# Performance work log

Measured on AMD Instinct MI355X. Metric: run time of the kernel, lower is better.

## Reference

```python
import jax, jax.numpy as jnp
import numpy as np

N_NODES = 50000
N_EDGES = 800000
IN_CH = 128
HIDDEN = 16
HEADS = 8
OUT_CH = 128
EDGE_DIM = 16


def _lin_params(key, fan_in, fan_out, bias=True):
    k1, k2 = jax.random.split(key)
    s = 1.0 / np.sqrt(fan_in)
    W = jax.random.uniform(k1, (fan_in, fan_out), jnp.float32, -s, s)
    if bias:
        b = jax.random.uniform(k2, (fan_out,), jnp.float32, -s, s)
        return W, b
    return W


def setup_inputs() -> dict:
    key = jax.random.key(0)
    ks = jax.random.split(key, 16)
    x = jax.random.normal(ks[0], (N_NODES, IN_CH), jnp.float32)
    edge_index = jax.random.randint(ks[1], (2, N_EDGES), 0, N_NODES, jnp.int64)
    edge_attr = jax.random.normal(ks[2], (N_EDGES, EDGE_DIM), jnp.float32)
    HC0 = HEADS * HIDDEN
    Wq0, bq0 = _lin_params(ks[3], IN_CH, HC0)
    Wk0, bk0 = _lin_params(ks[4], IN_CH, HC0)
    Wv0, bv0 = _lin_params(ks[5], IN_CH, HC0)
    We0 = _lin_params(ks[6], EDGE_DIM, HC0, bias=False)
    Ws0, bs0 = _lin_params(ks[7], IN_CH, HC0)
    Wq1, bq1 = _lin_params(ks[8], HC0, OUT_CH)
    Wk1, bk1 = _lin_params(ks[9], HC0, OUT_CH)
    Wv1, bv1 = _lin_params(ks[10], HC0, OUT_CH)
    We1 = _lin_params(ks[11], EDGE_DIM, OUT_CH, bias=False)
    Ws1, bs1 = _lin_params(ks[12], HC0, OUT_CH)
    return dict(x=x, edge_index=edge_index, edge_attr=edge_attr,
                Wq0=Wq0, bq0=bq0, Wk0=Wk0, bk0=bk0, Wv0=Wv0, bv0=bv0, We0=We0, Ws0=Ws0, bs0=bs0,
                Wq1=Wq1, bq1=bq1, Wk1=Wk1, bk1=bk1, Wv1=Wv1, bv1=bv1, We1=We1, Ws1=Ws1, bs1=bs1)


def transformer_conv(x, src, dst, edge_attr, Wq, bq, Wk, bk, Wv, bv, We, Ws, bs, heads, concat):
    """PyG TransformerConv: gather-attend-softmax(per dst)-scatter, edge features added to key/value."""
    N = x.shape[0]
    E = src.shape[0]
    C = Wq.shape[1] // heads
    q = (x @ Wq + bq).reshape(N, heads, C)
    k = (x @ Wk + bk).reshape(N, heads, C)
    v = (x @ Wv + bv).reshape(N, heads, C)
    e = (edge_attr @ We).reshape(E, heads, C)
    key_e = k[src] + e                                  # [E,H,C]
    alpha = jnp.sum(q[dst] * key_e, axis=-1) / jnp.sqrt(jnp.asarray(C, x.dtype))  # [E,H]
    # segment softmax over incoming edges of each dst node
    m = jax.ops.segment_max(alpha, dst, num_segments=N)       # [N,H]
    p = jnp.exp(alpha - m[dst])
    denom = jax.ops.segment_sum(p, dst, num_segments=N)       # [N,H]
    w = p / (denom[dst] + 1e-16)                              # [E,H]
    msg = (v[src] + e) * w[..., None]                         # [E,H,C]
    agg = jax.ops.segment_sum(msg.reshape(E, heads * C), dst, num_segments=N).reshape(N, heads, C)
    out = agg.reshape(N, heads * C) if concat else agg.mean(axis=1)
    return out + (x @ Ws + bs)                                # root skip connection


def reference(x, edge_index, edge_attr,
              Wq0, bq0, Wk0, bk0, Wv0, bv0, We0, Ws0, bs0,
              Wq1, bq1, Wk1, bk1, Wv1, bv1, We1, Ws1, bs1):
    src, dst = edge_index[0], edge_index[1]
    h = transformer_conv(x, src, dst, edge_attr, Wq0, bq0, Wk0, bk0, Wv0, bv0, We0, Ws0, bs0,
                         heads=HEADS, concat=True)
    h = jax.nn.relu(h)
    out = transformer_conv(h, src, dst, edge_attr, Wq1, bq1, Wk1, bk1, Wv1, bv1, We1, Ws1, bs1,
                           heads=1, concat=False)
    return out
```

## Files before the change

### kernel.cpp

```cpp
#include <hip/hip_runtime.h>
#include <stdint.h>

#define N_NODES 50000
#define N_EDGES 800000

typedef __bf16 bf16x8 __attribute__((ext_vector_type(8)));
typedef float f32x4 __attribute__((ext_vector_type(4)));

__device__ __forceinline__ unsigned short f2bf(float f) {
  union { float f; unsigned int i; } x; x.f = f;
  unsigned int i = x.i;
  unsigned int r = (i + 0x7fffu + ((i >> 16) & 1u)) >> 16;
  return (unsigned short)r;
}
__device__ __forceinline__ float bfl(unsigned int p) {
  union { unsigned int i; float f; } x; x.i = p << 16; return x.f;
}
__device__ __forceinline__ float bfh(unsigned int p) {
  union { unsigned int i; float f; } x; x.i = p & 0xffff0000u; return x.f;
}

struct Ptr8 { const float* p[8]; };

__global__ __launch_bounds__(256) void transpose_w(Ptr8 ws, unsigned short* wt) {
  int mat = blockIdx.x;
  const float* W = ws.p[mat];
  unsigned short* out = wt + mat * 16384;
  for (int it = 0; it < 64; ++it) {
    int idx = it * 256 + threadIdx.x;
    int n = idx >> 7, k = idx & 127;
    out[n * 128 + k] = f2bf(W[k * 128 + n]);
  }
}

__global__ void zero_kernel(int* cnt, int* cursor, int* srcpad, unsigned int* eapad) {
  int i = blockIdx.x * blockDim.x + threadIdx.x;
  if (i < N_NODES) { cnt[i] = 0; cursor[i] = 0; }
  if (i < 8)  srcpad[i] = 0;
  if (i < 64) eapad[i] = 0;
}

__global__ void hist_kernel(const int* __restrict__ dst, int* __restrict__ cnt) {
  int e = blockIdx.x * blockDim.x + threadIdx.x;
  if (e < N_EDGES) atomicAdd(&cnt[dst[e]], 1);
}

__global__ __launch_bounds__(1024) void scan_kernel(const int* __restrict__ cnt, int* __restrict__ rs) {
  const int n = N_NODES, per = 49;
  int t = threadIdx.x;
  int lo = t * per; int hi = lo + per;
  if (lo > n) lo = n;
  if (hi > n) hi = n;
  int s = 0;
  for (int i = lo; i < hi; ++i) s += cnt[i];
  int lane = t & 63, wv = t >> 6;
  int v = s;
  #pragma unroll
  for (int off = 1; off < 64; off <<= 1) {
    int u = __shfl_up(v, off, 64);
    if (lane >= off) v += u;
  }
  __shared__ int wsum[16], woff[16];
  if (lane == 63) wsum[wv] = v;
  __syncthreads();
  if (t == 0) { int a = 0; for (int w = 0; w < 16; ++w) { woff[w] = a; a += wsum[w]; } }
  __syncthreads();
  int run = woff[wv] + (v - s);
  if (t == 0) rs[0] = 0;
  for (int i = lo; i < hi; ++i) { run += cnt[i]; rs[i + 1] = run; }
}

__global__ void scatter_kernel(const int* __restrict__ src, const int* __restrict__ dst,
                               const int* __restrict__ rs, int* __restrict__ cursor,
                               int* __restrict__ srcArr, int* __restrict__ eidxArr) {
  int e = blockIdx.x * blockDim.x + threadIdx.x;
  if (e < N_EDGES) {
    int d = dst[e];
    int pos = rs[d] + atomicAdd(&cursor[d], 1);
    srcArr[pos]  = src[e];
    eidxArr[pos] = e;
  }
}

__global__ __launch_bounds__(256) void ea_gather(const float* __restrict__ EA,
                                                 const int* __restrict__ eidxArr,
                                                 unsigned short* __restrict__ eacsr) {
  int r = blockIdx.x * 32 + (threadIdx.x >> 3);
  if (r >= N_EDGES) return;
  int j = (threadIdx.x & 7) * 2;
  int e = eidxArr[r];
  float2 v = *(const float2*)(EA + (size_t)e * 16 + j);
  unsigned int pk = (unsigned int)f2bf(v.x) | ((unsigned int)f2bf(v.y) << 16);
  *(unsigned int*)(eacsr + (size_t)r * 16 + j) = pk;
}

struct Gemm4Args {
  const float* Xf;
  const unsigned short* Xh;
  const unsigned short* Wt;
  const float* b[4];
  unsigned short* o[4];
  int M;
};

template<bool XF32>
__global__ __launch_bounds__(256) void node_gemm4(Gemm4Args ga) {
  __shared__ alignas(16) unsigned short At[128 * 128];
  __shared__ alignas(16) unsigned short Bt[128 * 128];
  int m0 = blockIdx.x * 128;
  int lane = threadIdx.x & 63, wv = threadIdx.x >> 6;
  int wm = wv >> 1, wn = wv & 1;
  int lr = lane & 15, lk = lane >> 4;

  #pragma unroll
  for (int it = 0; it < 8; ++it) {
    int c = it * 256 + threadIdx.x;
    int row = c >> 4, slot = c & 15;
    int dsl = slot ^ (row & 7);
    int grow = m0 + row; if (grow >= ga.M) grow = ga.M - 1;
    alignas(16) unsigned short tmp[8];
    if (XF32) {
      const float* xp = ga.Xf + (size_t)grow * 128 + slot * 8;
      float4 a = *(const float4*)xp;
      float4 b = *(const float4*)(xp + 4);
      tmp[0] = f2bf(a.x); tmp[1] = f2bf(a.y); tmp[2] = f2bf(a.z); tmp[3] = f2bf(a.w);
      tmp[4] = f2bf(b.x); tmp[5] = f2bf(b.y); tmp[6] = f2bf(b.z); tmp[7] = f2bf(b.w);
    } else {
      *(uint4*)tmp = *(const uint4*)(ga.Xh + (size_t)grow * 128 + slot * 8);
    }
    *(uint4*)(&At[row * 128 + dsl * 8]) = *(const uint4*)tmp;
  }

  #pragma unroll
  for (int which = 0; which < 4; ++which) {
    if (which) __syncthreads();
    const unsigned short* Wt = ga.Wt + which * 16384;
    #pragma unroll
    for (int it = 0; it < 8; ++it) {
      int c = it * 256 + threadIdx.x;
      int row = c >> 4, slot = c & 15;
      int dsl = slot ^ (row & 7);
      *(uint4*)(&Bt[row * 128 + dsl * 8]) = *(const uint4*)(Wt + c * 8);
    }
    __syncthreads();

    f32x4 acc[4][4];
    #pragma unroll
    for (int mi = 0; mi < 4; ++mi)
      #pragma unroll
      for (int ni = 0; ni < 4; ++ni) acc[mi][ni] = (f32x4){0.f, 0.f, 0.f, 0.f};

    #pragma unroll
    for (int kk = 0; kk < 4; ++kk) {
      bf16x8 af[4], bfr[4];
      #pragma unroll
      for (int mi = 0; mi < 4; ++mi) {
        int row = wm * 64 + mi * 16 + lr;
        int slot = (kk * 4 + lk) ^ (row & 7);
        af[mi] = *(const bf16x8*)(&At[row * 128 + slot * 8]);
      }
      #pragma unroll
      for (int ni = 0; ni < 4; ++ni) {
        int row = wn * 64 + ni * 16 + lr;
        int slot = (kk * 4 + lk) ^ (row & 7);
        bfr[ni] = *(const bf16x8*)(&Bt[row * 128 + slot * 8]);
      }
      #pragma unroll
      for (int mi = 0; mi < 4; ++mi)
        #pragma unroll
        for (int ni = 0; ni < 4; ++ni)
          acc[mi][ni] = __builtin_amdgcn_mfma_f32_16x16x32_bf16(af[mi], bfr[ni], acc[mi][ni], 0, 0, 0);
    }

    const float* bias = ga.b[which];
    unsigned short* outp = ga.o[which];
    float bv[4];
    #pragma unroll
    for (int ni = 0; ni < 4; ++ni) bv[ni] = bias[wn * 64 + ni * 16 + lr];
    #pragma unroll
    for (int mi = 0; mi < 4; ++mi) {
      #pragma unroll
      for (int i = 0; i < 4; ++i) {
        int row = m0 + wm * 64 + mi * 16 + lk * 4 + i;
        if (row < ga.M) {
          #pragma unroll
          for (int ni = 0; ni < 4; ++ni) {
            int col = wn * 64 + ni * 16 + lr;
            outp[(size_t)row * 128 + col] = f2bf(acc[mi][ni][i] + bv[ni]);
          }
        }
      }
    }
  }
}

template<int CHALF, bool RELU, bool OUT_BF16>
__global__ __launch_bounds__(256) void edge_attn(
    const unsigned short* __restrict__ Q, const unsigned short* __restrict__ Kb,
    const unsigned short* __restrict__ Vb, const unsigned short* __restrict__ S,
    const float* __restrict__ We, const unsigned short* __restrict__ EAC,
    const int* __restrict__ srcArr, const int* __restrict__ rs,
    void* __restrict__ outv, float inv_sqrt_c) {
  int wv = threadIdx.x >> 6, lane = threadIdx.x & 63;
  int node = blockIdx.x * 4 + wv;
  if (node >= N_NODES) return;
  int c0 = lane * 2;
  int jbase = (lane & 1) * 8 + ((lane >> 1) & 1) * 4 + ((lane >> 2) & 1) * 2;

  unsigned int qp = *(const unsigned int*)(Q + (size_t)node * 128 + c0);
  unsigned int sp = *(const unsigned int*)(S + (size_t)node * 128 + c0);
  float qa = bfl(qp) * inv_sqrt_c;
  float qb = bfh(qp) * inv_sqrt_c;

  float part[16];
  #pragma unroll
  for (int j = 0; j < 16; ++j) {
    float2 wp = *(const float2*)(We + j * 128 + c0);
    part[j] = qa * wp.x + qb * wp.y;
  }
  {
    bool hi = lane & 1;
    #pragma unroll
    for (int j = 0; j < 8; ++j) {
      float kept = hi ? part[j + 8] : part[j];
      float sent = hi ? part[j] : part[j + 8];
      part[j] = kept + __shfl_xor(sent, 1, 64);
    }
    hi = lane & 2;
    #pragma unroll
    for (int j = 0; j < 4; ++j) {
      float kept = hi ? part[j + 4] : part[j];
      float sent = hi ? part[j] : part[j + 4];
      part[j] = kept + __shfl_xor(sent, 2, 64);
    }
    hi = lane & 4;
    #pragma unroll
    for (int j = 0; j < 2; ++j) {
      float kept = hi ? part[j + 2] : part[j];
      float sent = hi ? part[j] : part[j + 2];
      part[j] = kept + __shfl_xor(sent, 4, 64);
    }
  }
  if (CHALF == 64) {
    #pragma unroll
    for (int s = 8; s <= 32; s <<= 1) {
      part[0] += __shfl_xor(part[0], s, 64);
      part[1] += __shfl_xor(part[1], s, 64);
    }
  }
  float qw0 = part[0] * (CHALF == 64 ? 0.125f : 1.0f);
  float qw1 = part[1] * (CHALF == 64 ? 0.125f : 1.0f);

  int i0 = rs[node], i1 = rs[node + 1];
  int deg = i1 - i0;
  float den = 0.f, a0 = 0.f, a1 = 0.f, wea0 = 0.f, wea1 = 0.f;

  struct Buf { unsigned int kp[8], vp[8], ep[8]; };
  Buf bA, bB;
  int svA = 0, svB = 0;

  auto load_src = [&](int c) -> int {
    return srcArr[i0 + c * 8 + (lane & 7)];
  };
  auto gather = [&](Buf& b, int c, int sv) {
    #pragma unroll
    for (int j = 0; j < 8; ++j) {
      int s = __shfl(sv, j, 8);
      b.kp[j] = *(const unsigned int*)(Kb + (size_t)s * 128 + c0);
      b.vp[j] = *(const unsigned int*)(Vb + (size_t)s * 128 + c0);
      b.ep[j] = *(const unsigned int*)(EAC + (size_t)(i0 + c * 8 + j) * 16 + jbase);
    }
  };
  auto compute = [&](const Buf& b, int c) {
    #pragma unroll
    for (int j = 0; j < 8; ++j) {
      int g = i0 + c * 8 + j;
      float ea0 = bfl(b.ep[j]), ea1 = bfh(b.ep[j]);
      float p = qa * bfl(b.kp[j]) + qb * bfh(b.kp[j]) + qw0 * ea0 + qw1 * ea1;
      #pragma unroll
      for (int off = 1; off < CHALF; off <<= 1) p += __shfl_xor(p, off, 64);
      float w = (g < i1) ? __expf(p) : 0.f;
      den  += w;
      a0   += w * bfl(b.vp[j]);
      a1   += w * bfh(b.vp[j]);
      wea0 += w * ea0;
      wea1 += w * ea1;
    }
  };

  int nch = (deg + 7) >> 3;
  if (nch > 0) {
    svA = load_src(0);
    if (nch > 1) svB = load_src(1);
    gather(bA, 0, svA);
    int c = 0;
    while (true) {
      if (c + 1 < nch) gather(bB, c + 1, svB);
      if (c + 2 < nch) svA = load_src(c + 2);
      compute(bA, c);
      ++c; if (c >= nch) break;
      if (c + 1 < nch) gather(bA, c + 1, svA);
      if (c + 2 < nch) svB = load_src(c + 2);
      compute(bB, c);
      ++c; if (c >= nch) break;
    }
  }

  float inv = 1.f / (den + 1e-16f);
  float eadd0 = 0.f, eadd1 = 0.f;
  #pragma unroll
  for (int j = 0; j < 16; ++j) {
    int owner = ((j >> 3) & 1) | (((j >> 2) & 1) << 1) | (((j >> 1) & 1) << 2);
    int srcl = (lane & 56) | owner;
    float val = __shfl((j & 1) ? wea1 : wea0, srcl, 64);
    float2 wp = *(const float2*)(We + j * 128 + c0);
    eadd0 += val * wp.x;
    eadd1 += val * wp.y;
  }
  float o0 = (a0 + eadd0) * inv + bfl(sp);
  float o1 = (a1 + eadd1) * inv + bfh(sp);
  if (RELU) { o0 = fmaxf(o0, 0.f); o1 = fmaxf(o1, 0.f); }
  if (OUT_BF16) {
    unsigned int op = ((unsigned int)f2bf(o1) << 16) | (unsigned int)f2bf(o0);
    *(unsigned int*)((unsigned short*)outv + (size_t)node * 128 + c0) = op;
  } else {
    *(float2*)((float*)outv + (size_t)node * 128 + c0) = make_float2(o0, o1);
  }
}

extern "C" void kernel_launch(void* const* d_in, const int* in_sizes, int n_in,
                              void* d_out, int out_size, void* d_ws, size_t ws_size,
                              hipStream_t stream) {
  const float* x   = (const float*)d_in[0];
  const int*   ei  = (const int*)d_in[1];
  const float* ea  = (const float*)d_in[2];
  const float* Wq0 = (const float*)d_in[3];
  const float* bq0 = (const float*)d_in[4];
  const float* Wk0 = (const float*)d_in[5];
  const float* bk0 = (const float*)d_in[6];
  const float* Wv0 = (const float*)d_in[7];
  const float* bv0 = (const float*)d_in[8];
  const float* We0 = (const float*)d_in[9];
  const float* Ws0 = (const float*)d_in[10];
  const float* bs0 = (const float*)d_in[11];
  const float* Wq1 = (const float*)d_in[12];
  const float* bq1 = (const float*)d_in[13];
  const float* Wk1 = (const float*)d_in[14];
  const float* bk1 = (const float*)d_in[15];
  const float* Wv1 = (const float*)d_in[16];
  const float* bv1 = (const float*)d_in[17];
  const float* We1 = (const float*)d_in[18];
  const float* Ws1 = (const float*)d_in[19];
  const float* bs1 = (const float*)d_in[20];

  char* ws = (char*)d_ws;
  size_t off = 0;
  auto alloc = [&](size_t bytes) -> void* {
    void* p = ws + off;
    off = (off + bytes + 255) & ~(size_t)255;
    return p;
  };
  unsigned short* WT    = (unsigned short*)alloc(8 * 16384 * 2);
  unsigned short* q     = (unsigned short*)alloc((size_t)N_NODES * 128 * 2);
  unsigned short* k     = (unsigned short*)alloc((size_t)N_NODES * 128 * 2);
  unsigned short* v     = (unsigned short*)alloc((size_t)N_NODES * 128 * 2);
  unsigned short* s     = (unsigned short*)alloc((size_t)N_NODES * 128 * 2);
  unsigned short* h     = (unsigned short*)alloc((size_t)N_NODES * 128 * 2);
  unsigned short* eacsr = (unsigned short*)alloc(((size_t)N_EDGES + 8) * 16 * 2);
  int* cnt     = (int*)alloc(N_NODES * 4);
  int* rs      = (int*)alloc((N_NODES + 1) * 4);
  int* cursor  = (int*)alloc(N_NODES * 4);
  int* srcArr  = (int*)alloc(((size_t)N_EDGES + 8) * 4);
  int* eidxArr = (int*)alloc((size_t)N_EDGES * 4);

  const int* srcp = ei;
  const int* dstp = ei + N_EDGES;

  Ptr8 p8 = {{Wq0, Wk0, Wv0, Ws0, Wq1, Wk1, Wv1, Ws1}};
  transpose_w<<<8, 256, 0, stream>>>(p8, WT);
  zero_kernel<<<196, 256, 0, stream>>>(cnt, cursor, srcArr + N_EDGES,
                                       (unsigned int*)(eacsr + (size_t)N_EDGES * 16));
  hist_kernel<<<3125, 256, 0, stream>>>(dstp, cnt);
  scan_kernel<<<1, 1024, 0, stream>>>(cnt, rs);
  scatter_kernel<<<3125, 256, 0, stream>>>(srcp, dstp, rs, cursor, srcArr, eidxArr);
  ea_gather<<<25000, 256, 0, stream>>>(ea, eidxArr, eacsr);

  Gemm4Args ga0 = { x, nullptr, WT, {bq0, bk0, bv0, bs0}, {q, k, v, s}, N_NODES };
  node_gemm4<true><<<391, 256, 0, stream>>>(ga0);
  edge_attn<8, true, true><<<12500, 256, 0, stream>>>(q, k, v, s, We0, eacsr,
                                                      srcArr, rs, h, 0.25f);

  Gemm4Args ga1 = { nullptr, h, WT + 4 * 16384, {bq1, bk1, bv1, bs1}, {q, k, v, s}, N_NODES };
  node_gemm4<false><<<391, 256, 0, stream>>>(ga1);
  edge_attn<64, false, false><<<12500, 256, 0, stream>>>(q, k, v, s, We1, eacsr,
                                                         srcArr, rs, d_out, 0.08838834764831845f);
}
```

Measured before the change: 639.0 us.

## Interleave K/V rows, fuse edge-attr gather into scatter, persistent attention grid

The GEMM epilogue now writes K and V interleaved into one buffer, so each edge gather in the attention kernel is a single 8-byte load per lane instead of two 4-byte loads. Edge-attribute bf16 conversion is folded into the CSR scatter kernel, which removes the separate ea_gather pass and the eidx array. The zero kernel is replaced by memsets. The attention kernel becomes a grid-stride loop over 2048 blocks with an occupancy hint, and it moves the EA and S loads to later in the loop. The costs are scattered 2-byte stores in the GEMM epilogue and edge-attr loads that are no longer prefetched.

```diff
diff --git a/kernel.cpp b/kernel.cpp
--- a/kernel.cpp
+++ b/kernel.cpp
@@ -3,6 +3,7 @@
 
 #define N_NODES 50000
 #define N_EDGES 800000
+#define NGROUPS ((N_NODES + 3) / 4)
 
 typedef __bf16 bf16x8 __attribute__((ext_vector_type(8)));
 typedef float f32x4 __attribute__((ext_vector_type(4)));
@@ -12,6 +13,9 @@
   unsigned int i = x.i;
   unsigned int r = (i + 0x7fffu + ((i >> 16) & 1u)) >> 16;
   return (unsigned short)r;
+}
+__device__ __forceinline__ unsigned int pk2bf(float a, float b) {
+  return (unsigned int)f2bf(a) | ((unsigned int)f2bf(b) << 16);
 }
 __device__ __forceinline__ float bfl(unsigned int p) {
   union { unsigned int i; float f; } x; x.i = p << 16; return x.f;
@@ -31,13 +35,6 @@
     int n = idx >> 7, k = idx & 127;
     out[n * 128 + k] = f2bf(W[k * 128 + n]);
   }
-}
-
-__global__ void zero_kernel(int* cnt, int* cursor, int* srcpad, unsigned int* eapad) {
-  int i = blockIdx.x * blockDim.x + threadIdx.x;
-  if (i < N_NODES) { cnt[i] = 0; cursor[i] = 0; }
-  if (i < 8)  srcpad[i] = 0;
-  if (i < 64) eapad[i] = 0;
 }
 
 __global__ void hist_kernel(const int* __restrict__ dst, int* __restrict__ cnt) {
@@ -71,27 +68,21 @@
 }
 
 __global__ void scatter_kernel(const int* __restrict__ src, const int* __restrict__ dst,
+                               const float* __restrict__ EA,
                                const int* __restrict__ rs, int* __restrict__ cursor,
-                               int* __restrict__ srcArr, int* __restrict__ eidxArr) {
+                               int* __restrict__ srcArr, unsigned short* __restrict__ eacsr) {
   int e = blockIdx.x * blockDim.x + threadIdx.x;
   if (e < N_EDGES) {
     int d = dst[e];
     int pos = rs[d] + atomicAdd(&cursor[d], 1);
-    srcArr[pos]  = src[e];
-    eidxArr[pos] = e;
-  }
-}
-
-__global__ __launch_bounds__(256) void ea_gather(const float* __restrict__ EA,
-                                                 const int* __restrict__ eidxArr,
-                                                 unsigned short* __restrict__ eacsr) {
-  int r = blockIdx.x * 32 + (threadIdx.x >> 3);
-  if (r >= N_EDGES) return;
-  int j = (threadIdx.x & 7) * 2;
-  int e = eidxArr[r];
-  float2 v = *(const float2*)(EA + (size_t)e * 16 + j);
-  unsigned int pk = (unsigned int)f2bf(v.x) | ((unsigned int)f2bf(v.y) << 16);
-  *(unsigned int*)(eacsr + (size_t)r * 16 + j) = pk;
+    srcArr[pos] = src[e];
+    const float4* p = (const float4*)(EA + (size_t)e * 16);
+    float4 r0 = p[0], r1 = p[1], r2 = p[2], r3 = p[3];
+    uint4 u0 = { pk2bf(r0.x, r0.y), pk2bf(r0.z, r0.w), pk2bf(r1.x, r1.y), pk2bf(r1.z, r1.w) };
+    uint4 u1 = { pk2bf(r2.x, r2.y), pk2bf(r2.z, r2.w), pk2bf(r3.x, r3.y), pk2bf(r3.z, r3.w) };
+    *(uint4*)(eacsr + (size_t)pos * 16) = u0;
+    *(uint4*)(eacsr + (size_t)pos * 16 + 8) = u1;
+  }
 }
 
 struct Gemm4Args {
@@ -99,7 +90,9 @@
   const unsigned short* Xh;
   const unsigned short* Wt;
   const float* b[4];
-  unsigned short* o[4];
+  unsigned short* qb;
+  unsigned short* kvb;
+  unsigned short* sb;
   int M;
 };
 
@@ -173,7 +166,6 @@
     }
 
     const float* bias = ga.b[which];
-    unsigned short* outp = ga.o[which];
     float bv[4];
     #pragma unroll
     for (int ni = 0; ni < 4; ++ni) bv[ni] = bias[wn * 64 + ni * 16 + lr];
@@ -186,7 +178,10 @@
           #pragma unroll
           for (int ni = 0; ni < 4; ++ni) {
             int col = wn * 64 + ni * 16 + lr;
-            outp[(size_t)row * 128 + col] = f2bf(acc[mi][ni][i] + bv[ni]);
+            unsigned short val = f2bf(acc[mi][ni][i] + bv[ni]);
+            if (which == 0)      ga.qb[(size_t)row * 128 + col] = val;
+            else if (which == 3) ga.sb[(size_t)row * 128 + col] = val;
+            else ga.kvb[(size_t)row * 256 + (size_t)(col >> 1) * 4 + (col & 1) + (which == 2 ? 2 : 0)] = val;
           }
         }
       }
@@ -195,136 +190,138 @@
 }
 
 template<int CHALF, bool RELU, bool OUT_BF16>
-__global__ __launch_bounds__(256) void edge_attn(
-    const unsigned short* __restrict__ Q, const unsigned short* __restrict__ Kb,
-    const unsigned short* __restrict__ Vb, const unsigned short* __restrict__ S,
-    const float* __restrict__ We, const unsigned short* __restrict__ EAC,
+__global__ __launch_bounds__(256, 8) void edge_attn(
+    const unsigned short* __restrict__ Q, const uint2* __restrict__ KV,
+    const unsigned short* __restrict__ S, const float* __restrict__ We,
+    const unsigned short* __restrict__ EAC,
     const int* __restrict__ srcArr, const int* __restrict__ rs,
     void* __restrict__ outv, float inv_sqrt_c) {
   int wv = threadIdx.x >> 6, lane = threadIdx.x & 63;
-  int node = blockIdx.x * 4 + wv;
-  if (node >= N_NODES) return;
   int c0 = lane * 2;
   int jbase = (lane & 1) * 8 + ((lane >> 1) & 1) * 4 + ((lane >> 2) & 1) * 2;
 
-  unsigned int qp = *(const unsigned int*)(Q + (size_t)node * 128 + c0);
-  unsigned int sp = *(const unsigned int*)(S + (size_t)node * 128 + c0);
-  float qa = bfl(qp) * inv_sqrt_c;
-  float qb = bfh(qp) * inv_sqrt_c;
-
-  float part[16];
-  #pragma unroll
-  for (int j = 0; j < 16; ++j) {
-    float2 wp = *(const float2*)(We + j * 128 + c0);
-    part[j] = qa * wp.x + qb * wp.y;
-  }
-  {
-    bool hi = lane & 1;
-    #pragma unroll
-    for (int j = 0; j < 8; ++j) {
-      float kept = hi ? part[j + 8] : part[j];
-      float sent = hi ? part[j] : part[j + 8];
-      part[j] = kept + __shfl_xor(sent, 1, 64);
-    }
-    hi = lane & 2;
-    #pragma unroll
-    for (int j = 0; j < 4; ++j) {
-      float kept = hi ? part[j + 4] : part[j];
-      float sent = hi ? part[j] : part[j + 4];
-      part[j] = kept + __shfl_xor(sent, 2, 64);
-    }
-    hi = lane & 4;
-    #pragma unroll
-    for (int j = 0; j < 2; ++j) {
-      float kept = hi ? part[j + 2] : part[j];
-      float sent = hi ? part[j] : part[j + 2];
-      part[j] = kept + __shfl_xor(sent, 4, 64);
-    }
-  }
-  if (CHALF == 64) {
-    #pragma unroll
-    for (int s = 8; s <= 32; s <<= 1) {
-      part[0] += __shfl_xor(part[0], s, 64);
-      part[1] += __shfl_xor(part[1], s, 64);
-    }
-  }
-  float qw0 = part[0] * (CHALF == 64 ? 0.125f : 1.0f);
-  float qw1 = part[1] * (CHALF == 64 ? 0.125f : 1.0f);
-
-  int i0 = rs[node], i1 = rs[node + 1];
-  int deg = i1 - i0;
-  float den = 0.f, a0 = 0.f, a1 = 0.f, wea0 = 0.f, wea1 = 0.f;
-
-  struct Buf { unsigned int kp[8], vp[8], ep[8]; };
-  Buf bA, bB;
-  int svA = 0, svB = 0;
-
-  auto load_src = [&](int c) -> int {
-    return srcArr[i0 + c * 8 + (lane & 7)];
-  };
-  auto gather = [&](Buf& b, int c, int sv) {
-    #pragma unroll
-    for (int j = 0; j < 8; ++j) {
-      int s = __shfl(sv, j, 8);
-      b.kp[j] = *(const unsigned int*)(Kb + (size_t)s * 128 + c0);
-      b.vp[j] = *(const unsigned int*)(Vb + (size_t)s * 128 + c0);
-      b.ep[j] = *(const unsigned int*)(EAC + (size_t)(i0 + c * 8 + j) * 16 + jbase);
-    }
-  };
-  auto compute = [&](const Buf& b, int c) {
-    #pragma unroll
-    for (int j = 0; j < 8; ++j) {
-      int g = i0 + c * 8 + j;
-      float ea0 = bfl(b.ep[j]), ea1 = bfh(b.ep[j]);
-      float p = qa * bfl(b.kp[j]) + qb * bfh(b.kp[j]) + qw0 * ea0 + qw1 * ea1;
-      #pragma unroll
-      for (int off = 1; off < CHALF; off <<= 1) p += __shfl_xor(p, off, 64);
-      float w = (g < i1) ? __expf(p) : 0.f;
-      den  += w;
-      a0   += w * bfl(b.vp[j]);
-      a1   += w * bfh(b.vp[j]);
-      wea0 += w * ea0;
-      wea1 += w * ea1;
-    }
-  };
-
-  int nch = (deg + 7) >> 3;
-  if (nch > 0) {
-    svA = load_src(0);
-    if (nch > 1) svB = load_src(1);
-    gather(bA, 0, svA);
-    int c = 0;
-    while (true) {
-      if (c + 1 < nch) gather(bB, c + 1, svB);
-      if (c + 2 < nch) svA = load_src(c + 2);
-      compute(bA, c);
-      ++c; if (c >= nch) break;
-      if (c + 1 < nch) gather(bA, c + 1, svA);
-      if (c + 2 < nch) svB = load_src(c + 2);
-      compute(bB, c);
-      ++c; if (c >= nch) break;
-    }
-  }
-
-  float inv = 1.f / (den + 1e-16f);
-  float eadd0 = 0.f, eadd1 = 0.f;
-  #pragma unroll
-  for (int j = 0; j < 16; ++j) {
-    int owner = ((j >> 3) & 1) | (((j >> 2) & 1) << 1) | (((j >> 1) & 1) << 2);
-    int srcl = (lane & 56) | owner;
-    float val = __shfl((j & 1) ? wea1 : wea0, srcl, 64);
-    float2 wp = *(const float2*)(We + j * 128 + c0);
-    eadd0 += val * wp.x;
-    eadd1 += val * wp.y;
-  }
-  float o0 = (a0 + eadd0) * inv + bfl(sp);
-  float o1 = (a1 + eadd1) * inv + bfh(sp);
-  if (RELU) { o0 = fmaxf(o0, 0.f); o1 = fmaxf(o1, 0.f); }
-  if (OUT_BF16) {
-    unsigned int op = ((unsigned int)f2bf(o1) << 16) | (unsigned int)f2bf(o0);
-    *(unsigned int*)((unsigned short*)outv + (size_t)node * 128 + c0) = op;
-  } else {
-    *(float2*)((float*)outv + (size_t)node * 128 + c0) = make_float2(o0, o1);
+  for (int ng = blockIdx.x; ng < NGROUPS; ng += gridDim.x) {
+    int node = ng * 4 + wv;
+    if (node >= N_NODES) continue;
+
+    unsigned int qp = *(const unsigned int*)(Q + (size_t)node * 128 + c0);
+    float qa = bfl(qp) * inv_sqrt_c;
+    float qb = bfh(qp) * inv_sqrt_c;
+
+    float part[16];
+    #pragma unroll
+    for (int j = 0; j < 16; ++j) {
+      float2 wp = *(const float2*)(We + j * 128 + c0);
+      part[j] = qa * wp.x + qb * wp.y;
+    }
+    {
+      bool hi = lane & 1;
+      #pragma unroll
+      for (int j = 0; j < 8; ++j) {
+        float kept = hi ? part[j + 8] : part[j];
+        float sent = hi ? part[j] : part[j + 8];
+        part[j] = kept + __shfl_xor(sent, 1, 64);
+      }
+      hi = lane & 2;
+      #pragma unroll
+      for (int j = 0; j < 4; ++j) {
+        float kept = hi ? part[j + 4] : part[j];
+        float sent = hi ? part[j] : part[j + 4];
+        part[j] = kept + __shfl_xor(sent, 2, 64);
+      }
+      hi = lane & 4;
+      #pragma unroll
+      for (int j = 0; j < 2; ++j) {
+        float kept = hi ? part[j + 2] : part[j];
+        float sent = hi ? part[j] : part[j + 2];
+        part[j] = kept + __shfl_xor(sent, 4, 64);
+      }
+    }
+    if (CHALF == 64) {
+      #pragma unroll
+      for (int s = 8; s <= 32; s <<= 1) {
+        part[0] += __shfl_xor(part[0], s, 64);
+        part[1] += __shfl_xor(part[1], s, 64);
+      }
+    }
+    float qw0 = part[0] * (CHALF == 64 ? 0.125f : 1.0f);
+    float qw1 = part[1] * (CHALF == 64 ? 0.125f : 1.0f);
+
+    int i0 = rs[node], i1 = rs[node + 1];
+    int deg = i1 - i0;
+    float den = 0.f, a0 = 0.f, a1 = 0.f, wea0 = 0.f, wea1 = 0.f;
+
+    struct Buf { uint2 kv[8]; };
+    Buf bA, bB;
+    int svA = 0, svB = 0;
+
+    auto load_src = [&](int c) -> int {
+      return srcArr[i0 + c * 8 + (lane & 7)];
+    };
+    auto gather = [&](Buf& b, int sv) {
+      #pragma unroll
+      for (int j = 0; j < 8; ++j) {
+        int s = __shfl(sv, j, 8);
+        b.kv[j] = KV[(size_t)s * 64 + lane];
+      }
+    };
+    auto compute = [&](const Buf& b, int c) {
+      #pragma unroll
+      for (int j = 0; j < 8; ++j) {
+        int g = i0 + c * 8 + j;
+        unsigned int ep = *(const unsigned int*)(EAC + (size_t)g * 16 + jbase);
+        float ea0 = bfl(ep), ea1 = bfh(ep);
+        float p = qa * bfl(b.kv[j].x) + qb * bfh(b.kv[j].x) + qw0 * ea0 + qw1 * ea1;
+        #pragma unroll
+        for (int off = 1; off < CHALF; off <<= 1) p += __shfl_xor(p, off, 64);
+        float w = (g < i1) ? __expf(p) : 0.f;
+        den  += w;
+        a0   += w * bfl(b.kv[j].y);
+        a1   += w * bfh(b.kv[j].y);
+        wea0 += w * ea0;
+        wea1 += w * ea1;
+      }
+    };
+
+    int nch = (deg + 7) >> 3;
+    if (nch > 0) {
+      svA = load_src(0);
+      if (nch > 1) svB = load_src(1);
+      gather(bA, svA);
+      int c = 0;
+      while (true) {
+        if (c + 1 < nch) gather(bB, svB);
+        if (c + 2 < nch) svA = load_src(c + 2);
+        compute(bA, c);
+        ++c; if (c >= nch) break;
+        if (c + 1 < nch) gather(bA, svA);
+        if (c + 2 < nch) svB = load_src(c + 2);
+        compute(bB, c);
+        ++c; if (c >= nch) break;
+      }
+    }
+
+    float inv = 1.f / (den + 1e-16f);
+    float eadd0 = 0.f, eadd1 = 0.f;
+    #pragma unroll
+    for (int j = 0; j < 16; ++j) {
+      int owner = ((j >> 3) & 1) | (((j >> 2) & 1) << 1) | (((j >> 1) & 1) << 2);
+      int srcl = (lane & 56) | owner;
+      float val = __shfl((j & 1) ? wea1 : wea0, srcl, 64);
+      float2 wp = *(const float2*)(We + j * 128 + c0);
+      eadd0 += val * wp.x;
+      eadd1 += val * wp.y;
+    }
+    unsigned int sp = *(const unsigned int*)(S + (size_t)node * 128 + c0);
+    float o0 = (a0 + eadd0) * inv + bfl(sp);
+    float o1 = (a1 + eadd1) * inv + bfh(sp);
+    if (RELU) { o0 = fmaxf(o0, 0.f); o1 = fmaxf(o1, 0.f); }
+    if (OUT_BF16) {
+      unsigned int op = ((unsigned int)f2bf(o1) << 16) | (unsigned int)f2bf(o0);
+      *(unsigned int*)((unsigned short*)outv + (size_t)node * 128 + c0) = op;
+    } else {
+      *(float2*)((float*)outv + (size_t)node * 128 + c0) = make_float2(o0, o1);
+    }
   }
 }
 
@@ -362,36 +359,35 @@
   };
   unsigned short* WT    = (unsigned short*)alloc(8 * 16384 * 2);
   unsigned short* q     = (unsigned short*)alloc((size_t)N_NODES * 128 * 2);
-  unsigned short* k     = (unsigned short*)alloc((size_t)N_NODES * 128 * 2);
-  unsigned short* v     = (unsigned short*)alloc((size_t)N_NODES * 128 * 2);
+  unsigned short* kvb   = (unsigned short*)alloc((size_t)N_NODES * 256 * 2);
   unsigned short* s     = (unsigned short*)alloc((size_t)N_NODES * 128 * 2);
   unsigned short* h     = (unsigned short*)alloc((size_t)N_NODES * 128 * 2);
   unsigned short* eacsr = (unsigned short*)alloc(((size_t)N_EDGES + 8) * 16 * 2);
-  int* cnt     = (int*)alloc(N_NODES * 4);
-  int* rs      = (int*)alloc((N_NODES + 1) * 4);
-  int* cursor  = (int*)alloc(N_NODES * 4);
-  int* srcArr  = (int*)alloc(((size_t)N_EDGES + 8) * 4);
-  int* eidxArr = (int*)alloc((size_t)N_EDGES * 4);
+  int* cc     = (int*)alloc((size_t)2 * N_NODES * 4);
+  int* rs     = (int*)alloc((N_NODES + 1) * 4);
+  int* srcArr = (int*)alloc(((size_t)N_EDGES + 8) * 4);
+  int* cnt = cc, *cursor = cc + N_NODES;
 
   const int* srcp = ei;
   const int* dstp = ei + N_EDGES;
 
+  hipMemsetAsync(cc, 0, (size_t)2 * N_NODES * 4, stream);
+  hipMemsetAsync(srcArr + N_EDGES, 0, 8 * 4, stream);
+  hipMemsetAsync(eacsr + (size_t)N_EDGES * 16, 0, 8 * 16 * 2, stream);
+
   Ptr8 p8 = {{Wq0, Wk0, Wv0, Ws0, Wq1, Wk1, Wv1, Ws1}};
   transpose_w<<<8, 256, 0, stream>>>(p8, WT);
-  zero_kernel<<<196, 256, 0, stream>>>(cnt, cursor, srcArr + N_EDGES,
-                                       (unsigned int*)(eacsr + (size_t)N_EDGES * 16));
   hist_kernel<<<3125, 256, 0, stream>>>(dstp, cnt);
   scan_kernel<<<1, 1024, 0, stream>>>(cnt, rs);
-  scatter_kernel<<<3125, 256, 0, stream>>>(srcp, dstp, rs, cursor, srcArr, eidxArr);
-  ea_gather<<<25000, 256, 0, stream>>>(ea, eidxArr, eacsr);
-
-  Gemm4Args ga0 = { x, nullptr, WT, {bq0, bk0, bv0, bs0}, {q, k, v, s}, N_NODES };
+  scatter_kernel<<<3125, 256, 0, stream>>>(srcp, dstp, ea, rs, cursor, srcArr, eacsr);
+
+  Gemm4Args ga0 = { x, nullptr, WT, {bq0, bk0, bv0, bs0}, q, kvb, s, N_NODES };
   node_gemm4<true><<<391, 256, 0, stream>>>(ga0);
-  edge_attn<8, true, true><<<12500, 256, 0, stream>>>(q, k, v, s, We0, eacsr,
-                                                      srcArr, rs, h, 0.25f);
-
-  Gemm4Args ga1 = { nullptr, h, WT + 4 * 16384, {bq1, bk1, bv1, bs1}, {q, k, v, s}, N_NODES };
+  edge_attn<8, true, true><<<2048, 256, 0, stream>>>(q, (const uint2*)kvb, s, We0, eacsr,
+                                                     srcArr, rs, h, 0.25f);
+
+  Gemm4Args ga1 = { nullptr, h, WT + 4 * 16384, {bq1, bk1, bv1, bs1}, q, kvb, s, N_NODES };
   node_gemm4<false><<<391, 256, 0, stream>>>(ga1);
-  edge_attn<64, false, false><<<12500, 256, 0, stream>>>(q, k, v, s, We1, eacsr,
-                                                         srcArr, rs, d_out, 0.08838834764831845f);
-}
+  edge_attn<64, false, false><<<2048, 256, 0, stream>>>(q, (const uint2*)kvb, s, We1, eacsr,
+                                                        srcArr, rs, d_out, 0.08838834764831845f);
+}
```

Result: slower. 986.4 us (+54.4%).
